# Kernel tuning notes

Hardware: AMD Instinct MI355X
Metric: run time of the kernel (lower is better)

The kernel has to match this reference:

```python
import jax, jax.numpy as jnp
import numpy as np
import math

B, T, N_EMBED, HEAD = 8, 2048, 1024, 128

def setup_inputs() -> dict:
    key = jax.random.key(0)
    k1, k2, k3, k4 = jax.random.split(key, 4)
    index = jax.random.normal(k1, (B, T, N_EMBED), dtype=jnp.float32)
    # Linear weights stored as [in, out] for x @ W (torch stores [out,in]; math identical)
    scale = 1.0 / math.sqrt(N_EMBED)
    Wq = jax.random.normal(k2, (N_EMBED, HEAD), dtype=jnp.float32) * scale
    Wk = jax.random.normal(k3, (N_EMBED, HEAD), dtype=jnp.float32) * scale
    Wv = jax.random.normal(k4, (N_EMBED, HEAD), dtype=jnp.float32) * scale
    return {"index": index, "Wq": Wq, "Wk": Wk, "Wv": Wv}

def reference(index, Wq, Wk, Wv):
    Bsz, Tlen, C = index.shape
    q = index @ Wq  # [B,T,H]
    k = index @ Wk  # [B,T,H]
    v = index @ Wv  # [B,T,H]
    # NOTE: source scales by 1/sqrt(C) where C = n_embed (input channels)
    w = jnp.einsum('bth,bsh->bts', q, k) / jnp.sqrt(jnp.asarray(C, dtype=index.dtype))
    causal = jnp.tril(jnp.ones((Tlen, Tlen), dtype=bool))
    w = jnp.where(causal, w, -jnp.inf)
    w = jax.nn.softmax(w, axis=-1)
    out = jnp.einsum('bts,bsh->bth', w, v)  # [B,T,H]
    return out
```

## Files before the change

kernel.cpp:

```cpp
#include <hip/hip_runtime.h>
#include <hip/hip_bf16.h>


typedef __attribute__((ext_vector_type(8))) short bf16x8;
typedef __attribute__((ext_vector_type(4))) float f32x4;
typedef __attribute__((ext_vector_type(4))) int i32x4;

#define TB 8
#define TT 2048
#define TC 1024
#define TH 128
#define LOG2E 1.4426950408889634f
#define NEGBIG (-1e30f)
#define RESCALE_THR 8.0f

__device__ __forceinline__ float fexp2(float x) {
#if __has_builtin(__builtin_amdgcn_exp2f)
  return __builtin_amdgcn_exp2f(x);
#else
  return exp2f(x);
#endif
}
__device__ __forceinline__ float eexp(float y) { return fexp2(y * LOG2E); }

__device__ __forceinline__ short bf16s(float a) {
  __hip_bfloat16 h = __float2bfloat16(a);
  return *reinterpret_cast<short*>(&h);
}
__device__ __forceinline__ unsigned pk2(float a, float b) {
  float2 t; t.x = a; t.y = b;
  __hip_bfloat162 h = __float22bfloat162_rn(t);
  return *reinterpret_cast<unsigned*>(&h);
}

__global__ void wprep(const float* __restrict__ wq, const float* __restrict__ wk,
                      const float* __restrict__ wv, short* __restrict__ wt) {
  int id = blockIdx.x * 256 + threadIdx.x;
  int w = id >> 17;
  int r = id & 131071;
  int n = r >> 10, k = r & 1023;
  const float* src = (w == 0) ? wq : (w == 1) ? wk : wv;
  float v = src[k * TH + n];
  if (w == 0) v *= 0.03125f;
  wt[id] = bf16s(v);
}

__global__ __launch_bounds__(256, 3) void qkv_gemm(
    const float* __restrict__ x, const short* __restrict__ wt,
    short* __restrict__ qb, short* __restrict__ kb, short* __restrict__ vt) {
  __shared__ __align__(16) short lA[64 * 72];
  __shared__ __align__(16) short lB[128 * 72];
  int phys = blockIdx.x;
  int logical = (phys & 7) * 96 + (phys >> 3);
  int rt = logical / 3, w = logical - rt * 3;
  int row0 = rt << 6;
  const short* wsel = wt + w * (TH * TC);
  int tid = threadIdx.x;
  int lane = tid & 63;
  int wid = tid >> 6;
  int wr = wid >> 1, wc = wid & 1;
  int l15 = lane & 15, g = lane >> 4;
  f32x4 zero = {0.f, 0.f, 0.f, 0.f};
  f32x4 acc[2][4];
#pragma unroll
  for (int i = 0; i < 2; i++)
#pragma unroll
    for (int jj = 0; jj < 4; jj++) acc[i][jj] = zero;

  for (int k0 = 0; k0 < TC; k0 += 64) {
    __syncthreads();
#pragma unroll
    for (int rep = 0; rep < 4; rep++) {
      int idx = rep * 256 + tid;
      int r = idx >> 4, c4 = (idx & 15) << 2;
      float4 v = *reinterpret_cast<const float4*>(x + (size_t)(row0 + r) * TC + k0 + c4);
      uint2 u; u.x = pk2(v.x, v.y); u.y = pk2(v.z, v.w);
      *reinterpret_cast<uint2*>(&lA[r * 72 + c4]) = u;
    }
#pragma unroll
    for (int rep = 0; rep < 4; rep++) {
      int idx = rep * 256 + tid;
      int n = idx >> 3, c8 = (idx & 7) << 3;
      *reinterpret_cast<int4*>(&lB[n * 72 + c8]) =
          *reinterpret_cast<const int4*>(wsel + (size_t)n * TC + k0 + c8);
    }
    __syncthreads();
#pragma unroll
    for (int ks = 0; ks < 2; ks++) {
      bf16x8 a[2], b[4];
#pragma unroll
      for (int mf = 0; mf < 2; mf++)
        a[mf] = *reinterpret_cast<const bf16x8*>(&lA[(wr * 32 + mf * 16 + l15) * 72 + ks * 32 + g * 8]);
#pragma unroll
      for (int nf = 0; nf < 4; nf++)
        b[nf] = *reinterpret_cast<const bf16x8*>(&lB[(wc * 64 + nf * 16 + l15) * 72 + ks * 32 + g * 8]);
#pragma unroll
      for (int mf = 0; mf < 2; mf++)
#pragma unroll
        for (int nf = 0; nf < 4; nf++)
          acc[mf][nf] = __builtin_amdgcn_mfma_f32_16x16x32_bf16(a[mf], b[nf], acc[mf][nf], 0, 0, 0);
    }
  }
#pragma unroll
  for (int mf = 0; mf < 2; mf++)
#pragma unroll
    for (int nf = 0; nf < 4; nf++)
#pragma unroll
      for (int r = 0; r < 4; r++) {
        int m = row0 + wr * 32 + mf * 16 + g * 4 + r;
        int n = wc * 64 + nf * 16 + l15;
        short hv = bf16s(acc[mf][nf][r]);
        if (w == 0) qb[(size_t)m * TH + n] = hv;
        else if (w == 1) kb[(size_t)m * TH + n] = hv;
        else {
          int bb = m >> 11, t = m & 2047;
          vt[((size_t)bb * TH + n) * TT + t] = hv;
        }
      }
}

__global__ __launch_bounds__(256, 2) void attn(
    const short* __restrict__ qb, const short* __restrict__ kb,
    const short* __restrict__ vt, float* __restrict__ out) {
  __shared__ float buf[4 * 32 * 128];
  __shared__ float cm[4][32];
  __shared__ float cl[4][32];
  __shared__ float linv[32];
  int tid = threadIdx.x;
  int lane = tid & 63, wv = tid >> 6;
  int l15 = lane & 15, g = lane >> 4;
  int bid = blockIdx.x;
  int b = bid & 7;
  int s_ = bid >> 3;
  int qt = (bid < 256) ? (63 - s_) : (s_ - 32);
  int q0 = qt << 5;

  bf16x8 qfr[2][4];
  const short* qrow = qb + ((size_t)(b * TT + q0 + l15)) * TH + g * 8;
#pragma unroll
  for (int qf = 0; qf < 2; qf++)
#pragma unroll
    for (int ks = 0; ks < 4; ks++)
      qfr[qf][ks] = *reinterpret_cast<const bf16x8*>(qrow + (size_t)qf * 16 * TH + ks * 32);

  f32x4 zero = {0.f, 0.f, 0.f, 0.f};
  f32x4 acc[2][8];
#pragma unroll
  for (int qf = 0; qf < 2; qf++)
#pragma unroll
    for (int hf = 0; hf < 8; hf++) acc[qf][hf] = zero;
  float m_r[2] = {NEGBIG, NEGBIG};
  float l_r[2] = {0.f, 0.f};

  int lim = q0 + 31 - wv * 32;
  int nj = (lim >= 0) ? (lim >> 7) + 1 : 0;
  const short* kbase = kb + ((size_t)b * TT) * TH;
  const short* vbase = vt + ((size_t)b * TH) * TT;

  for (int j = 0; j < nj; j++) {
    int kv0 = j * 128 + wv * 32;
    bf16x8 kfr[2][4];
#pragma unroll
    for (int kvf = 0; kvf < 2; kvf++)
#pragma unroll
      for (int ks = 0; ks < 4; ks++)
        kfr[kvf][ks] = *reinterpret_cast<const bf16x8*>(
            kbase + (size_t)(kv0 + kvf * 16 + l15) * TH + ks * 32 + g * 8);
    bf16x8 vfr[8];
#pragma unroll
    for (int hf = 0; hf < 8; hf++)
      vfr[hf] = *reinterpret_cast<const bf16x8*>(
          vbase + (size_t)(hf * 16 + l15) * TT + kv0 + g * 8);

    f32x4 s[2][2];
    s[0][0] = zero; s[0][1] = zero; s[1][0] = zero; s[1][1] = zero;
    __builtin_amdgcn_s_setprio(1);
#pragma unroll
    for (int ks = 0; ks < 4; ks++)
#pragma unroll
      for (int kvf = 0; kvf < 2; kvf++)
#pragma unroll
        for (int qf = 0; qf < 2; qf++)
          s[kvf][qf] = __builtin_amdgcn_mfma_f32_16x16x32_bf16(
              kfr[kvf][ks], qfr[qf][ks], s[kvf][qf], 0, 0, 0);
    __builtin_amdgcn_s_setprio(0);

    float mm[2];
#pragma unroll
    for (int qf = 0; qf < 2; qf++) {
      int qg = q0 + qf * 16 + l15;
      float t = NEGBIG;
#pragma unroll
      for (int kvf = 0; kvf < 2; kvf++)
#pragma unroll
        for (int r = 0; r < 4; r++) {
          int kvg = kv0 + kvf * 16 + g * 4 + r;
          float v = s[kvf][qf][r];
          v = (kvg > qg) ? NEGBIG : v;
          s[kvf][qf][r] = v;
          t = fmaxf(t, v);
        }
      t = fmaxf(t, __shfl_xor(t, 16));
      t = fmaxf(t, __shfl_xor(t, 32));
      mm[qf] = t;
    }
    bool skip = __all((mm[0] - m_r[0] <= RESCALE_THR) &&
                      (mm[1] - m_r[1] <= RESCALE_THR));
    if (!skip) {
#pragma unroll
      for (int qf = 0; qf < 2; qf++) {
        float mn = fmaxf(m_r[qf], mm[qf]);
        float al = eexp(m_r[qf] - mn);
        m_r[qf] = mn;
        l_r[qf] *= al;
#pragma unroll
        for (int r = 0; r < 4; r++) {
          float av = __shfl(al, g * 4 + r);
#pragma unroll
          for (int hf = 0; hf < 8; hf++) acc[qf][hf][r] *= av;
        }
      }
    }
#pragma unroll
    for (int qf = 0; qf < 2; qf++) {
      float pv0 = eexp(s[0][qf][0] - m_r[qf]);
      float pv1 = eexp(s[0][qf][1] - m_r[qf]);
      float pv2 = eexp(s[0][qf][2] - m_r[qf]);
      float pv3 = eexp(s[0][qf][3] - m_r[qf]);
      float pw0 = eexp(s[1][qf][0] - m_r[qf]);
      float pw1 = eexp(s[1][qf][1] - m_r[qf]);
      float pw2 = eexp(s[1][qf][2] - m_r[qf]);
      float pw3 = eexp(s[1][qf][3] - m_r[qf]);
      float ps = ((pv0 + pv1) + (pv2 + pv3)) + ((pw0 + pw1) + (pw2 + pw3));
      ps += __shfl_xor(ps, 16);
      ps += __shfl_xor(ps, 32);
      l_r[qf] += ps;
      unsigned d0 = pk2(pv0, pv1), d1 = pk2(pv2, pv3);
      unsigned e0 = pk2(pw0, pw1), e1 = pk2(pw2, pw3);
      int lA_ = l15 + ((g & 1) << 5);
      int lB_ = lA_ + 16;
      int xa0 = __shfl((int)d0, lA_), xe0 = __shfl((int)e0, lA_);
      int xa1 = __shfl((int)d1, lA_), xe1 = __shfl((int)e1, lA_);
      int ya0 = __shfl((int)d0, lB_), ye0 = __shfl((int)e0, lB_);
      int ya1 = __shfl((int)d1, lB_), ye1 = __shfl((int)e1, lB_);
      bool hi = (g >= 2);
      i32x4 fr;
      fr.x = hi ? xe0 : xa0;
      fr.y = hi ? xe1 : xa1;
      fr.z = hi ? ye0 : ya0;
      fr.w = hi ? ye1 : ya1;
      bf16x8 pa = *reinterpret_cast<bf16x8*>(&fr);
      __builtin_amdgcn_s_setprio(1);
#pragma unroll
      for (int hf = 0; hf < 8; hf++)
        acc[qf][hf] = __builtin_amdgcn_mfma_f32_16x16x32_bf16(pa, vfr[hf], acc[qf][hf], 0, 0, 0);
      __builtin_amdgcn_s_setprio(0);
    }
  }

  if (g == 0) {
    cm[wv][l15] = m_r[0]; cm[wv][16 + l15] = m_r[1];
    cl[wv][l15] = l_r[0]; cl[wv][16 + l15] = l_r[1];
  }
  __syncthreads();
  float wgt[2];
#pragma unroll
  for (int qf = 0; qf < 2; qf++) {
    int ql = qf * 16 + l15;
    float M = fmaxf(fmaxf(cm[0][ql], cm[1][ql]), fmaxf(cm[2][ql], cm[3][ql]));
    wgt[qf] = eexp(m_r[qf] - M);
    if (wv == 0 && g == 0) {
      float lt = 0.f;
#pragma unroll
      for (int t = 0; t < 4; t++)
        lt += eexp(cm[t][ql] - M) * cl[t][ql];
      linv[ql] = 1.0f / lt;
    }
  }
#pragma unroll
  for (int qf = 0; qf < 2; qf++)
#pragma unroll
    for (int r = 0; r < 4; r++) {
      float w_ = __shfl(wgt[qf], g * 4 + r);
      int row = qf * 16 + g * 4 + r;
#pragma unroll
      for (int hf = 0; hf < 8; hf++)
        buf[(wv * 32 + row) * 128 + hf * 16 + l15] = acc[qf][hf][r] * w_;
    }
  __syncthreads();
#pragma unroll
  for (int rep = 0; rep < 4; rep++) {
    int row = wv * 8 + rep * 2 + (lane >> 5);
    int col = (lane & 31) * 4;
    f32x4 sum = *reinterpret_cast<f32x4*>(&buf[row * 128 + col]);
#pragma unroll
    for (int t = 1; t < 4; t++)
      sum += *reinterpret_cast<f32x4*>(&buf[(t * 32 + row) * 128 + col]);
    float li = linv[row];
    f32x4 o = sum * li;
    *reinterpret_cast<f32x4*>(&out[((size_t)(b * TT + q0 + row)) * TH + col]) = o;
  }
}

extern "C" void kernel_launch(void* const* d_in, const int* in_sizes, int n_in,
                              void* d_out, int out_size, void* d_ws, size_t ws_size,
                              hipStream_t stream) {
  const float* x  = (const float*)d_in[0];
  const float* wq = (const float*)d_in[1];
  const float* wk = (const float*)d_in[2];
  const float* wv = (const float*)d_in[3];
  float* out = (float*)d_out;
  char* ws = (char*)d_ws;
  short* qb = (short*)(ws);
  short* kb = (short*)(ws + (size_t)(4u << 20));
  short* vt = (short*)(ws + (size_t)(8u << 20));
  short* wt = (short*)(ws + (size_t)(12u << 20));

  wprep<<<1536, 256, 0, stream>>>(wq, wk, wv, wt);
  qkv_gemm<<<768, 256, 0, stream>>>(x, wt, qb, kb, vt);
  attn<<<512, 256, 0, stream>>>(qb, kb, vt, out);
}
```

Measured before the change: 189.3 us.

## Load QKV GEMM operands directly from global memory, dropping LDS staging

```diff
diff --git a/kernel.cpp b/kernel.cpp
--- a/kernel.cpp
+++ b/kernel.cpp
@@ -48,8 +48,6 @@
 __global__ __launch_bounds__(256, 3) void qkv_gemm(
     const float* __restrict__ x, const short* __restrict__ wt,
     short* __restrict__ qb, short* __restrict__ kb, short* __restrict__ vt) {
-  __shared__ __align__(16) short lA[64 * 72];
-  __shared__ __align__(16) short lB[128 * 72];
   int phys = blockIdx.x;
   int logical = (phys & 7) * 96 + (phys >> 3);
   int rt = logical / 3, w = logical - rt * 3;
@@ -60,6 +58,7 @@
   int wid = tid >> 6;
   int wr = wid >> 1, wc = wid & 1;
   int l15 = lane & 15, g = lane >> 4;
+
   f32x4 zero = {0.f, 0.f, 0.f, 0.f};
   f32x4 acc[2][4];
 #pragma unroll
@@ -67,33 +66,28 @@
 #pragma unroll
     for (int jj = 0; jj < 4; jj++) acc[i][jj] = zero;
 
+  const float* arow = x + (size_t)(row0 + wr * 32 + l15) * TC + g * 8;
+  const short* brow = wsel + (size_t)(wc * 64 + l15) * TC + g * 8;
+
+#pragma unroll 2
   for (int k0 = 0; k0 < TC; k0 += 64) {
-    __syncthreads();
-#pragma unroll
-    for (int rep = 0; rep < 4; rep++) {
-      int idx = rep * 256 + tid;
-      int r = idx >> 4, c4 = (idx & 15) << 2;
-      float4 v = *reinterpret_cast<const float4*>(x + (size_t)(row0 + r) * TC + k0 + c4);
-      uint2 u; u.x = pk2(v.x, v.y); u.y = pk2(v.z, v.w);
-      *reinterpret_cast<uint2*>(&lA[r * 72 + c4]) = u;
-    }
-#pragma unroll
-    for (int rep = 0; rep < 4; rep++) {
-      int idx = rep * 256 + tid;
-      int n = idx >> 3, c8 = (idx & 7) << 3;
-      *reinterpret_cast<int4*>(&lB[n * 72 + c8]) =
-          *reinterpret_cast<const int4*>(wsel + (size_t)n * TC + k0 + c8);
-    }
-    __syncthreads();
 #pragma unroll
     for (int ks = 0; ks < 2; ks++) {
+      int ko = k0 + ks * 32;
       bf16x8 a[2], b[4];
 #pragma unroll
-      for (int mf = 0; mf < 2; mf++)
-        a[mf] = *reinterpret_cast<const bf16x8*>(&lA[(wr * 32 + mf * 16 + l15) * 72 + ks * 32 + g * 8]);
+      for (int mf = 0; mf < 2; mf++) {
+        const float* p = arow + (size_t)mf * 16 * TC + ko;
+        float4 lo = *reinterpret_cast<const float4*>(p);
+        float4 hi = *reinterpret_cast<const float4*>(p + 4);
+        union { bf16x8 v; unsigned u[4]; } pkk;
+        pkk.u[0] = pk2(lo.x, lo.y); pkk.u[1] = pk2(lo.z, lo.w);
+        pkk.u[2] = pk2(hi.x, hi.y); pkk.u[3] = pk2(hi.z, hi.w);
+        a[mf] = pkk.v;
+      }
 #pragma unroll
       for (int nf = 0; nf < 4; nf++)
-        b[nf] = *reinterpret_cast<const bf16x8*>(&lB[(wc * 64 + nf * 16 + l15) * 72 + ks * 32 + g * 8]);
+        b[nf] = *reinterpret_cast<const bf16x8*>(brow + (size_t)nf * 16 * TC + ko);
 #pragma unroll
       for (int mf = 0; mf < 2; mf++)
 #pragma unroll
```

Measured after the change: 218.9 us. 1.16x slower.
